# Kernel tuning notes

Measured on AMD Instinct MI355X. Metric: run time of the kernel, lower is better.

## Reference

```python
import jax, jax.numpy as jnp
import numpy as np

N = 4_194_304
NUM_ITER = 6
DAMPING = 0.95
TOL = 1e-06
EPS = 1e-12


def _translate_x(dx):
    """4x4 homogeneous translation along the optical (x) axis."""
    return jnp.eye(4, dtype=dx.dtype).at[0, 3].set(dx)


def setup_inputs() -> dict:
    key = jax.random.key(0)
    k1, k2, k3 = jax.random.split(key, 3)
    # Ray origins: near x = -10, transverse spread within/around the aperture
    px = -10.0 + 0.5 * jax.random.normal(k1, (N, 1), dtype=jnp.float32)
    pyz = 8.0 * jax.random.normal(k2, (N, 2), dtype=jnp.float32)
    P = jnp.concatenate([px, pyz], axis=-1)
    # Ray directions: mostly +x, small transverse components, normalized
    vyz = 0.05 * jax.random.normal(k3, (N, 2), dtype=jnp.float32)
    V = jnp.concatenate([jnp.ones((N, 1), jnp.float32), vyz], axis=-1)
    V = V / jnp.linalg.norm(V, axis=-1, keepdims=True)
    tf = jnp.eye(4, dtype=jnp.float32)
    return {
        "P": P,
        "V": V,
        "tf": tf,
        "diameter": jnp.float32(50.0),
        "C": jnp.float32(0.02),
        "anchors": jnp.zeros((2,), jnp.float32),
        "scale": jnp.float32(1.0),
        "normalize": jnp.asarray(False),
    }


def reference(P, V, tf, diameter, C, anchors, scale, normalize):
    # normalize: curvature interpreted relative to semi-diameter
    C_eff = jnp.where(normalize, C * 2.0 / diameter, C)
    s2 = scale * scale

    def sag(r2):  # scaled spherical sag: f = scale * g(r2/scale^2)
        u = r2 / s2
        root = jnp.sqrt(jnp.clip(1.0 - C_eff * C_eff * u, EPS))
        return scale * C_eff * u / (1.0 + root)

    def sag_grad(y, z):  # (df/dy, df/dz) = C*(y,z) / (scale*sqrt(1-C^2 u))
        u = (y * y + z * z) / s2
        root = jnp.sqrt(jnp.clip(1.0 - C_eff * C_eff * u, EPS))
        k = C_eff / (scale * root)
        return k * y, k * z

    # anchors shift the surface along x by fractions of the edge sag (extent)
    extent = sag(jnp.square(diameter * 0.5))
    surface_tf = tf @ _translate_x(-anchors[0] * extent)
    next_tf = tf @ _translate_x((anchors[1] - anchors[0]) * extent)

    # Rays into surface-local frame
    R = surface_tf[:3, :3]
    tv = surface_tf[:3, 3]
    Pl = (P - tv) @ R  # [N,3] = R^T (P - t)
    Vl = V @ R
    vx, vy, vz = Vl[:, 0], Vl[:, 1], Vl[:, 2]

    safe_vx = jnp.where(jnp.abs(vx) > EPS, vx, EPS)
    t = -Pl[:, 0] / safe_vx  # init: intersection with plane x=0

    # Damped Newton on F(t) = sag(y(t),z(t)) - x(t)
    for _ in range(NUM_ITER):
        p = Pl + t[:, None] * Vl
        y, z = p[:, 1], p[:, 2]
        F = sag(y * y + z * z) - p[:, 0]
        gy, gz = sag_grad(y, z)
        dF = gy * vy + gz * vz - vx
        dF = jnp.where(jnp.abs(dF) > EPS, dF, EPS)
        t = t - DAMPING * F / dF

    p = Pl + t[:, None] * Vl
    y, z = p[:, 1], p[:, 2]
    r2 = y * y + z * z
    F = sag(r2) - p[:, 0]
    gy, gz = sag_grad(y, z)
    # implicit-surface normal: grad(sag(y,z) - x) = (-1, gy, gz), normalized
    n_local = jnp.stack([-jnp.ones_like(gy), gy, gz], axis=-1)
    n_local = n_local / jnp.linalg.norm(n_local, axis=-1, keepdims=True)
    normals = n_local @ R.T  # back to global frame

    valid = (r2 <= jnp.square(diameter * 0.5)) & (jnp.abs(F) < 100.0 * TOL)
    return t, normals, valid, surface_tf, next_tf
```

## Files before the change

### kernel.cpp

```cpp
#include <hip/hip_runtime.h>

#define F_EPS 1e-12f
#define F_DAMPING 0.95f
#define N_ITER 6
#define TPB 256
#define RPT 4
#define TILE (TPB * RPT)
#define TILES 2

__launch_bounds__(TPB)
__global__ void trace_kernel(const float* __restrict__ P,
                             const float* __restrict__ V,
                             const float* __restrict__ tf,
                             const float* __restrict__ diameter,
                             const float* __restrict__ Cc,
                             const float* __restrict__ anchors,
                             const float* __restrict__ scale_p,
                             const unsigned char* __restrict__ normalize,
                             float* __restrict__ out,
                             int n)
{
    const int tid = threadIdx.x;

    float R0,R1,R2,R3,R4,R5,R6,R7,R8, tv0,tv1,tv2;
    float C_eff, scale, half_d2, inv_s2;
    {
#pragma clang fp contract(off)
        float d  = diameter[0];
        float c  = Cc[0];
        float sc = scale_p[0];
        bool  nrm = (normalize[0] != 0);
        C_eff = nrm ? (c * 2.0f / d) : c;
        float s2 = sc * sc;
        float hr = d * 0.5f;
        half_d2 = hr * hr;
        float u = half_d2 / s2;
        float root = sqrtf(fmaxf(1.0f - (C_eff * C_eff) * u, F_EPS));
        float extent = sc * C_eff * u / (1.0f + root);
        float a0 = anchors[0], a1 = anchors[1];
        float dx0 = -a0 * extent;
        float dx1 = (a1 - a0) * extent;
        R0 = tf[0]; R1 = tf[1]; R2 = tf[2];
        R3 = tf[4]; R4 = tf[5]; R5 = tf[6];
        R6 = tf[8]; R7 = tf[9]; R8 = tf[10];
        tv0 = tf[0] * dx0 + tf[3];
        tv1 = tf[4] * dx0 + tf[7];
        tv2 = tf[8] * dx0 + tf[11];
        scale  = sc;
        inv_s2 = 1.0f / s2;
        if (blockIdx.x == 0 && tid < 16) {
            int i = tid >> 2, j = tid & 3;
            float v  = tf[tid];
            float sv = (j == 3) ? (tf[i * 4] * dx0 + v) : v;
            float nv = (j == 3) ? (tf[i * 4] * dx1 + v) : v;
            float* out_tail = out + (size_t)n * 5;
            out_tail[tid]      = sv;
            out_tail[16 + tid] = nv;
        }
    }
    const float ce2   = C_eff * C_eff;
    const float sC    = scale * C_eff;
    const float a_num = sC * inv_s2;
    const float ce2s  = ce2 * inv_s2;
    const float Cs    = C_eff / scale;

    float* t_out = out;
    float* n_out = out + (size_t)n;
    float* v_out = out + (size_t)n * 4;

    const float4* P4 = reinterpret_cast<const float4*>(P);
    const float4* V4 = reinterpret_cast<const float4*>(V);
    float4*       N4 = reinterpret_cast<float4*>(n_out);

    const int total_full = n / TILE;
    const int tile0 = blockIdx.x * TILES;

    auto process = [&](float4 p0, float4 p1, float4 p2,
                       float4 q0, float4 q1, float4 q2, int tile) {
        float Px[4], Py[4], Pz[4], Vx[4], Vy[4], Vz[4];
        Px[0]=p0.x; Py[0]=p0.y; Pz[0]=p0.z; Px[1]=p0.w; Py[1]=p1.x; Pz[1]=p1.y;
        Px[2]=p1.z; Py[2]=p1.w; Pz[2]=p2.x; Px[3]=p2.y; Py[3]=p2.z; Pz[3]=p2.w;
        Vx[0]=q0.x; Vy[0]=q0.y; Vz[0]=q0.z; Vx[1]=q0.w; Vy[1]=q1.x; Vz[1]=q1.y;
        Vx[2]=q1.z; Vy[2]=q1.w; Vz[2]=q2.x; Vx[3]=q2.y; Vy[3]=q2.z; Vz[3]=q2.w;

        float Plx[4], Ply[4], Plz[4], vx[4], vy[4], vz[4], tN[4];
#pragma unroll
        for (int r = 0; r < 4; ++r) {
            float px0 = Px[r] - tv0, py0 = Py[r] - tv1, pz0 = Pz[r] - tv2;
            Plx[r] = px0 * R0 + py0 * R3 + pz0 * R6;
            Ply[r] = px0 * R1 + py0 * R4 + pz0 * R7;
            Plz[r] = px0 * R2 + py0 * R5 + pz0 * R8;
            vx[r] = Vx[r] * R0 + Vy[r] * R3 + Vz[r] * R6;
            vy[r] = Vx[r] * R1 + Vy[r] * R4 + Vz[r] * R7;
            vz[r] = Vx[r] * R2 + Vy[r] * R5 + Vz[r] * R8;
            float safe_vx = (fabsf(vx[r]) > F_EPS) ? vx[r] : F_EPS;
            tN[r] = (-Plx[r]) * __builtin_amdgcn_rcpf(safe_vx);
        }

#pragma unroll
        for (int it = 0; it < N_ITER; ++it) {
#pragma unroll
            for (int r = 0; r < 4; ++r) {
                float pxx = fmaf(tN[r], vx[r], Plx[r]);
                float py  = fmaf(tN[r], vy[r], Ply[r]);
                float pz  = fmaf(tN[r], vz[r], Plz[r]);
                float r2  = fmaf(py, py, pz * pz);
                float m   = fmaxf(fmaf(-ce2s, r2, 1.0f), F_EPS);
                float rsq = __builtin_amdgcn_rsqf(m);
                float root = m * rsq;
                float k    = Cs * rsq;
                float ird  = __builtin_amdgcn_rcpf(1.0f + root);
                float F    = fmaf(a_num * r2, ird, -pxx);
                float dF = fmaf(k * py, vy[r], fmaf(k * pz, vz[r], -vx[r]));
                dF = (fabsf(dF) > F_EPS) ? dF : F_EPS;
                tN[r] = fmaf(-F_DAMPING * F, __builtin_amdgcn_rcpf(dF), tN[r]);
            }
        }

        float tres[4], nxo[4], nyo[4], nzo[4], val[4];
#pragma unroll
        for (int r = 0; r < 4; ++r) {
            float pxx = fmaf(tN[r], vx[r], Plx[r]);
            float py  = fmaf(tN[r], vy[r], Ply[r]);
            float pz  = fmaf(tN[r], vz[r], Plz[r]);
            float r2  = fmaf(py, py, pz * pz);
            float m   = fmaxf(fmaf(-ce2s, r2, 1.0f), F_EPS);
            float rsq = __builtin_amdgcn_rsqf(m);
            float root = m * rsq;
            float k    = Cs * rsq;
            float ird  = __builtin_amdgcn_rcpf(1.0f + root);
            float F    = fmaf(a_num * r2, ird, -pxx);
            float gy = k * py, gz = k * pz;
            float nn2 = fmaf(gy, gy, fmaf(gz, gz, 1.0f));
            float irn = __builtin_amdgcn_rsqf(nn2);
            float nlx = -irn, nly = gy * irn, nlz = gz * irn;
            nxo[r] = nlx * R0 + nly * R1 + nlz * R2;
            nyo[r] = nlx * R3 + nly * R4 + nlz * R5;
            nzo[r] = nlx * R6 + nly * R7 + nlz * R8;
            tres[r] = tN[r];
            val[r]  = ((r2 <= half_d2) && (fabsf(F) < 1e-4f)) ? 1.0f : 0.0f;
        }

        int base = tile * TILE + 4 * tid;
        *reinterpret_cast<float4*>(t_out + base) = make_float4(tres[0], tres[1], tres[2], tres[3]);
        *reinterpret_cast<float4*>(v_out + base) = make_float4(val[0], val[1], val[2], val[3]);
        size_t f4 = (size_t)tile * (TILE * 3 / 4) + 3 * tid;
        N4[f4]     = make_float4(nxo[0], nyo[0], nzo[0], nxo[1]);
        N4[f4 + 1] = make_float4(nyo[1], nzo[1], nxo[2], nyo[2]);
        N4[f4 + 2] = make_float4(nzo[2], nxo[3], nyo[3], nzo[3]);
    };

    float4 c0, c1, c2, c3, c4, c5;
    float4 x0, x1, x2, x3, x4, x5;

#define LOADT(T, a0, a1, a2, b0, b1, b2)                         \
    do {                                                         \
        size_t f4_ = (size_t)(T) * (TILE * 3 / 4) + 3 * tid;     \
        a0 = P4[f4_]; a1 = P4[f4_ + 1]; a2 = P4[f4_ + 2];        \
        b0 = V4[f4_]; b1 = V4[f4_ + 1]; b2 = V4[f4_ + 2];        \
    } while (0)

    if (tile0 < total_full) {
        LOADT(tile0, c0, c1, c2, c3, c4, c5);
#pragma unroll
        for (int k = 0; k < TILES; ++k) {
            int tile = tile0 + k;
            if (tile >= total_full) break;
            bool have_next = (k + 1 < TILES) && (tile + 1 < total_full);
            if (have_next) LOADT(tile + 1, x0, x1, x2, x3, x4, x5);
            process(c0, c1, c2, c3, c4, c5, tile);
            if (have_next) { c0 = x0; c1 = x1; c2 = x2; c3 = x3; c4 = x4; c5 = x5; }
        }
    }
#undef LOADT

    const int rem = n - total_full * TILE;
    if (rem > 0 && total_full >= tile0 && total_full < tile0 + TILES) {
        const int start = total_full * TILE;
        for (int r = 0; r < RPT; ++r) {
            int i = start + tid * RPT + r;
            if (i >= n) break;
            float Pxs = P[(size_t)i * 3 + 0], Pys = P[(size_t)i * 3 + 1], Pzs = P[(size_t)i * 3 + 2];
            float Vxs = V[(size_t)i * 3 + 0], Vys = V[(size_t)i * 3 + 1], Vzs = V[(size_t)i * 3 + 2];
            float px0 = Pxs - tv0, py0 = Pys - tv1, pz0 = Pzs - tv2;
            float Plx = px0 * R0 + py0 * R3 + pz0 * R6;
            float Ply = px0 * R1 + py0 * R4 + pz0 * R7;
            float Plz = px0 * R2 + py0 * R5 + pz0 * R8;
            float vx = Vxs * R0 + Vys * R3 + Vzs * R6;
            float vy = Vxs * R1 + Vys * R4 + Vzs * R7;
            float vz = Vxs * R2 + Vys * R5 + Vzs * R8;
            float safe_vx = (fabsf(vx) > F_EPS) ? vx : F_EPS;
            float tN = (-Plx) * __builtin_amdgcn_rcpf(safe_vx);
#pragma unroll
            for (int it = 0; it < N_ITER; ++it) {
                float pxx = fmaf(tN, vx, Plx);
                float py  = fmaf(tN, vy, Ply);
                float pz  = fmaf(tN, vz, Plz);
                float r2  = fmaf(py, py, pz * pz);
                float m   = fmaxf(fmaf(-ce2s, r2, 1.0f), F_EPS);
                float rsq = __builtin_amdgcn_rsqf(m);
                float root = m * rsq;
                float k    = Cs * rsq;
                float ird  = __builtin_amdgcn_rcpf(1.0f + root);
                float F    = fmaf(a_num * r2, ird, -pxx);
                float dF = fmaf(k * py, vy, fmaf(k * pz, vz, -vx));
                dF = (fabsf(dF) > F_EPS) ? dF : F_EPS;
                tN = fmaf(-F_DAMPING * F, __builtin_amdgcn_rcpf(dF), tN);
            }
            float pxx = fmaf(tN, vx, Plx);
            float py  = fmaf(tN, vy, Ply);
            float pz  = fmaf(tN, vz, Plz);
            float r2  = fmaf(py, py, pz * pz);
            float m   = fmaxf(fmaf(-ce2s, r2, 1.0f), F_EPS);
            float rsq = __builtin_amdgcn_rsqf(m);
            float root = m * rsq;
            float k    = Cs * rsq;
            float ird  = __builtin_amdgcn_rcpf(1.0f + root);
            float F    = fmaf(a_num * r2, ird, -pxx);
            float gy = k * py, gz = k * pz;
            float nn2 = fmaf(gy, gy, fmaf(gz, gz, 1.0f));
            float irn = __builtin_amdgcn_rsqf(nn2);
            float nlx = -irn, nly = gy * irn, nlz = gz * irn;
            t_out[i] = tN;
            n_out[(size_t)i * 3 + 0] = nlx * R0 + nly * R1 + nlz * R2;
            n_out[(size_t)i * 3 + 1] = nlx * R3 + nly * R4 + nlz * R5;
            n_out[(size_t)i * 3 + 2] = nlx * R6 + nly * R7 + nlz * R8;
            v_out[i] = ((r2 <= half_d2) && (fabsf(F) < 1e-4f)) ? 1.0f : 0.0f;
        }
    }
}

extern "C" void kernel_launch(void* const* d_in, const int* in_sizes, int n_in,
                              void* d_out, int out_size, void* d_ws, size_t ws_size,
                              hipStream_t stream) {
    const float* P  = (const float*)d_in[0];
    const float* V  = (const float*)d_in[1];
    const float* tf = (const float*)d_in[2];
    const float* diameter = (const float*)d_in[3];
    const float* C  = (const float*)d_in[4];
    const float* anchors = (const float*)d_in[5];
    const float* scale = (const float*)d_in[6];
    const unsigned char* normalize = (const unsigned char*)d_in[7];
    int n = in_sizes[0] / 3;
    float* out = (float*)d_out;

    int total_tiles = (n + TILE - 1) / TILE;
    int blocks = (total_tiles + TILES - 1) / TILES;
    if (blocks < 1) blocks = 1;
    trace_kernel<<<blocks, TPB, 0, stream>>>(P, V, tf, diameter, C, anchors, scale,
                                             normalize, out, n);
}
```

Measured before the change: 178.5 us.

## Process one tile per block with nontemporal stores and higher occupancy bound

Drops the two-tile-per-block software prefetch loop so each block handles a single tile, which doubles the grid size. Output stores become nontemporal vector stores so write-once results do not pollute the cache, and the launch bounds now request 10 waves per SIMD to push occupancy up. The trade is losing explicit load/compute overlap within a block in exchange for more concurrent blocks hiding latency, with a risk of register pressure from the tighter launch bound.

Result: no change. 180.6 us (+1.2%).

```diff
diff --git a/kernel.cpp b/kernel.cpp
--- a/kernel.cpp
+++ b/kernel.cpp
@@ -6,9 +6,14 @@
 #define TPB 256
 #define RPT 4
 #define TILE (TPB * RPT)
-#define TILES 2
-
-__launch_bounds__(TPB)
+
+typedef float f32x4 __attribute__((ext_vector_type(4)));
+static __device__ __forceinline__ void nt_store4(float* p, float a, float b, float c, float d) {
+    f32x4 v = {a, b, c, d};
+    __builtin_nontemporal_store(v, reinterpret_cast<f32x4*>(p));
+}
+
+__launch_bounds__(TPB, 10)
 __global__ void trace_kernel(const float* __restrict__ P,
                              const float* __restrict__ V,
                              const float* __restrict__ tf,
@@ -68,15 +73,17 @@
     float* n_out = out + (size_t)n;
     float* v_out = out + (size_t)n * 4;
 
-    const float4* P4 = reinterpret_cast<const float4*>(P);
-    const float4* V4 = reinterpret_cast<const float4*>(V);
-    float4*       N4 = reinterpret_cast<float4*>(n_out);
-
     const int total_full = n / TILE;
-    const int tile0 = blockIdx.x * TILES;
-
-    auto process = [&](float4 p0, float4 p1, float4 p2,
-                       float4 q0, float4 q1, float4 q2, int tile) {
+    const int tile = blockIdx.x;
+
+    if (tile < total_full) {
+        const float4* P4 = reinterpret_cast<const float4*>(P);
+        const float4* V4 = reinterpret_cast<const float4*>(V);
+
+        const size_t f4 = (size_t)tile * (TILE * 3 / 4) + 3 * tid;
+        float4 p0 = P4[f4], p1 = P4[f4 + 1], p2 = P4[f4 + 2];
+        float4 q0 = V4[f4], q1 = V4[f4 + 1], q2 = V4[f4 + 2];
+
         float Px[4], Py[4], Pz[4], Vx[4], Vy[4], Vz[4];
         Px[0]=p0.x; Py[0]=p0.y; Pz[0]=p0.z; Px[1]=p0.w; Py[1]=p1.x; Pz[1]=p1.y;
         Px[2]=p1.z; Py[2]=p1.w; Pz[2]=p2.x; Px[3]=p2.y; Py[3]=p2.z; Pz[3]=p2.w;
@@ -141,41 +148,14 @@
             val[r]  = ((r2 <= half_d2) && (fabsf(F) < 1e-4f)) ? 1.0f : 0.0f;
         }
 
-        int base = tile * TILE + 4 * tid;
-        *reinterpret_cast<float4*>(t_out + base) = make_float4(tres[0], tres[1], tres[2], tres[3]);
-        *reinterpret_cast<float4*>(v_out + base) = make_float4(val[0], val[1], val[2], val[3]);
-        size_t f4 = (size_t)tile * (TILE * 3 / 4) + 3 * tid;
-        N4[f4]     = make_float4(nxo[0], nyo[0], nzo[0], nxo[1]);
-        N4[f4 + 1] = make_float4(nyo[1], nzo[1], nxo[2], nyo[2]);
-        N4[f4 + 2] = make_float4(nzo[2], nxo[3], nyo[3], nzo[3]);
-    };
-
-    float4 c0, c1, c2, c3, c4, c5;
-    float4 x0, x1, x2, x3, x4, x5;
-
-#define LOADT(T, a0, a1, a2, b0, b1, b2)                         \
-    do {                                                         \
-        size_t f4_ = (size_t)(T) * (TILE * 3 / 4) + 3 * tid;     \
-        a0 = P4[f4_]; a1 = P4[f4_ + 1]; a2 = P4[f4_ + 2];        \
-        b0 = V4[f4_]; b1 = V4[f4_ + 1]; b2 = V4[f4_ + 2];        \
-    } while (0)
-
-    if (tile0 < total_full) {
-        LOADT(tile0, c0, c1, c2, c3, c4, c5);
-#pragma unroll
-        for (int k = 0; k < TILES; ++k) {
-            int tile = tile0 + k;
-            if (tile >= total_full) break;
-            bool have_next = (k + 1 < TILES) && (tile + 1 < total_full);
-            if (have_next) LOADT(tile + 1, x0, x1, x2, x3, x4, x5);
-            process(c0, c1, c2, c3, c4, c5, tile);
-            if (have_next) { c0 = x0; c1 = x1; c2 = x2; c3 = x3; c4 = x4; c5 = x5; }
-        }
-    }
-#undef LOADT
-
-    const int rem = n - total_full * TILE;
-    if (rem > 0 && total_full >= tile0 && total_full < tile0 + TILES) {
+        const int base = tile * TILE + 4 * tid;
+        nt_store4(t_out + base, tres[0], tres[1], tres[2], tres[3]);
+        nt_store4(v_out + base, val[0], val[1], val[2], val[3]);
+        float* nb = n_out + f4 * 4;
+        nt_store4(nb,      nxo[0], nyo[0], nzo[0], nxo[1]);
+        nt_store4(nb + 4,  nyo[1], nzo[1], nxo[2], nyo[2]);
+        nt_store4(nb + 8,  nzo[2], nxo[3], nyo[3], nzo[3]);
+    } else {
         const int start = total_full * TILE;
         for (int r = 0; r < RPT; ++r) {
             int i = start + tid * RPT + r;
@@ -244,8 +224,7 @@
     int n = in_sizes[0] / 3;
     float* out = (float*)d_out;
 
-    int total_tiles = (n + TILE - 1) / TILE;
-    int blocks = (total_tiles + TILES - 1) / TILES;
+    int blocks = (n + TILE - 1) / TILE;
     if (blocks < 1) blocks = 1;
     trace_kernel<<<blocks, TPB, 0, stream>>>(P, V, tf, diameter, C, anchors, scale,
                                              normalize, out, n);
```
